# Optimization experiments

Measured on AMD Instinct MI355X. Metric: run time of the kernel, lower is better.

The kernel has to match this reference:

```python
import math
import jax, jax.numpy as jnp
import numpy as np

_INIT_LOG_GAIN = math.log(5.0)
B, L, D = 4, 1024, 256


def setup_inputs() -> dict:
    key = jax.random.key(0)
    kq, kk = jax.random.split(key)
    q = jax.random.normal(kq, (B, L, D), dtype=jnp.float32)
    k = jax.random.normal(kk, (B, L, D), dtype=jnp.float32)
    P_prev = jnp.zeros((B, D, D), dtype=jnp.float32)
    log_gain = jnp.full((D,), _INIT_LOG_GAIN, dtype=jnp.float32)
    output_scale = jnp.ones((D,), dtype=jnp.float32)
    return {"q": q, "k": k, "P_prev": P_prev, "log_gain": log_gain,
            "output_scale": output_scale}


def reference(q, k, P_prev, log_gain, output_scale):
    """Sequential rank-1 projection-state update + normalized matvec + gated tanh.

    q, k: [B, L, D]; P_prev: [B, D, D]. Returns (q_out [B,L,D], P_final [B,D,D]).
    """
    gain = jnp.exp(log_gain)  # effective gain, [D]

    def step(P, qk_t):
        q_t, k_t = qk_t                                   # each [B, D]
        P = P + jnp.einsum('bi,bj->bij', k_t, k_t)        # rank-1 update
        fro = jnp.sqrt(jnp.sum(P * P, axis=(-2, -1), keepdims=True))
        P_norm = P / (fro + 1e-7)
        q_aligned = jnp.einsum('bij,bj->bi', P_norm, q_t)
        q_safe = jnp.tanh(gain * q_aligned) * output_scale
        return P, q_safe

    # scan over the L time axis
    P_final, outs = jax.lax.scan(step, P_prev,
                                 (jnp.swapaxes(q, 0, 1), jnp.swapaxes(k, 0, 1)))
    q_out = jnp.swapaxes(outs, 0, 1)  # [B, L, D]
    return q_out, P_final
```

## Files before the change

kernel.cpp:

```cpp
#include <hip/hip_runtime.h>
#include <math.h>


#define LDSPAD 68

typedef __attribute__((ext_vector_type(8))) short bf16x8;
typedef __attribute__((ext_vector_type(4))) float f32x4;

__device__ __forceinline__ unsigned short f2bf(float x) {
    union { float f; unsigned u; } c; c.f = x;
    return (unsigned short)((c.u + (0x7fffu + ((c.u >> 16) & 1u))) >> 16);
}
__device__ __forceinline__ unsigned f2bf2(float a, float b) {
    union { float f; unsigned u; } ca, cb; ca.f = a; cb.f = b;
    unsigned ua = ca.u + (0x7fffu + ((ca.u >> 16) & 1u));
    unsigned ub = cb.u + (0x7fffu + ((cb.u >> 16) & 1u));
    return (ua >> 16) | (ub & 0xffff0000u);
}
__device__ __forceinline__ void gload16(const unsigned short* g, const unsigned short* l) {
    __builtin_amdgcn_global_load_lds(
        (const __attribute__((address_space(1))) unsigned int*)g,
        (__attribute__((address_space(3))) unsigned int*)l, 16, 0, 0);
}
__device__ __forceinline__ bf16x8 ldsfrag(const unsigned short* lds, int row0, int g0, int lane) {
    int r = row0 + (lane & 15);
    int g = g0 + (lane >> 4);
    return *(const bf16x8*)(lds + r * 64 + (((g ^ (r & 7)) & 7) << 3));
}
#define MFMA16(a, b, c) __builtin_amdgcn_mfma_f32_16x16x32_bf16(a, b, c, 0, 0, 0)

__global__ __launch_bounds__(256) void k_prep(
    const float* __restrict__ Q, const float* __restrict__ K,
    unsigned short* __restrict__ Qb, unsigned short* __restrict__ Kb)
{
    size_t e = ((size_t)blockIdx.x * 256 + threadIdx.x) * 8;
    float4 a0 = *(const float4*)(Q + e), a1 = *(const float4*)(Q + e + 4);
    float4 b0 = *(const float4*)(K + e), b1 = *(const float4*)(K + e + 4);
    uint4 qo = {f2bf2(a0.x, a0.y), f2bf2(a0.z, a0.w), f2bf2(a1.x, a1.y), f2bf2(a1.z, a1.w)};
    uint4 ko = {f2bf2(b0.x, b0.y), f2bf2(b0.z, b0.w), f2bf2(b1.x, b1.y), f2bf2(b1.z, b1.w)};
    *(uint4*)(Qb + e) = qo;
    *(uint4*)(Kb + e) = ko;
}

__global__ __launch_bounds__(256) void k_gsp(
    const unsigned short* __restrict__ Qb, const unsigned short* __restrict__ Kb,
    const float* __restrict__ K, const float* __restrict__ Pprev,
    unsigned short* __restrict__ Sc, float* __restrict__ r2d, float* __restrict__ P4,
    unsigned short* __restrict__ KT, float* __restrict__ basePart,
    int B_, int L, int D, int nT, int nPairs)
{
    __shared__ unsigned short smem[24576];
    int tid = threadIdx.x, lane = tid & 63, w = tid >> 6;
    int fr = lane & 15, fq = lane >> 4;
    int nDt = D >> 6, nLt = L >> 6;
    int nGS = B_ * nPairs;
    int nP4 = B_ * nDt * nDt * 4;
    int nKT = B_ * nLt * nDt;
    int bx = blockIdx.x;
    int id = (bx < nGS) ? ((bx & 7) * (nGS >> 3) + (bx >> 3)) : bx;

    if (id < nGS) {
        int p = id % nPairs;
        int b = id / nPairs;
        int ti = (int)((sqrtf(8.f * p + 1.f) - 1.f) * 0.5f);
        while ((ti + 1) * (ti + 2) / 2 <= p) ti++;
        while (ti * (ti + 1) / 2 > p) ti--;
        int sj = p - ti * (ti + 1) / 2;

        const unsigned short* Qp = Qb + (size_t)b * L * D;
        const unsigned short* Kp = Kb + (size_t)b * L * D;
        int t0 = ti * 64, s0 = sj * 64;
        int wr = w >> 1, wc = w & 1;

        f32x4 g00 = {0,0,0,0}, g01 = {0,0,0,0}, g10 = {0,0,0,0}, g11 = {0,0,0,0};
        f32x4 s00 = {0,0,0,0}, s01 = {0,0,0,0}, s10 = {0,0,0,0}, s11 = {0,0,0,0};

        auto STAGE = [&](int ck, int bo) {
            const unsigned short* Kt = Kp + (size_t)t0 * D + ck * 64;
            const unsigned short* Qt = Qp + (size_t)t0 * D + ck * 64;
            const unsigned short* Ks = Kp + (size_t)s0 * D + ck * 64;
            for (int c = w; c < 8; c += 4) {
                int lrow = c * 8 + (lane >> 3);
                int gof = lrow * D + ((((lane & 7) ^ (lrow & 7)) & 7) << 3);
                gload16(Kt + gof, smem + bo + c * 512);
                gload16(Qt + gof, smem + bo + 4096 + c * 512);
                gload16(Ks + gof, smem + bo + 8192 + c * 512);
            }
        };

        STAGE(0, 0);
        __syncthreads();
        for (int ck = 0; ck < 4; ck++) {
            int cur = (ck & 1) * 12288;
            if (ck < 3) STAGE(ck + 1, 12288 - cur);
            const unsigned short* Kt = smem + cur;
            const unsigned short* Qt = Kt + 4096;
            const unsigned short* Ks = Kt + 8192;
#pragma unroll
            for (int kc = 0; kc < 2; kc++) {
                bf16x8 bK0 = ldsfrag(Ks, wc * 32, kc * 4, lane);
                bf16x8 bK1 = ldsfrag(Ks, wc * 32 + 16, kc * 4, lane);
                bf16x8 aK0 = ldsfrag(Kt, wr * 32, kc * 4, lane);
                bf16x8 aK1 = ldsfrag(Kt, wr * 32 + 16, kc * 4, lane);
                bf16x8 aQ0 = ldsfrag(Qt, wr * 32, kc * 4, lane);
                bf16x8 aQ1 = ldsfrag(Qt, wr * 32 + 16, kc * 4, lane);
                g00 = MFMA16(aK0, bK0, g00);
                g01 = MFMA16(aK0, bK1, g01);
                g10 = MFMA16(aK1, bK0, g10);
                g11 = MFMA16(aK1, bK1, g11);
                s00 = MFMA16(aQ0, bK0, s00);
                s01 = MFMA16(aQ0, bK1, s01);
                s10 = MFMA16(aQ1, bK0, s10);
                s11 = MFMA16(aQ1, bK1, s11);
            }
            __syncthreads();
        }

        float rsv[2][4] = {{0, 0, 0, 0}, {0, 0, 0, 0}};
#define EPI(MI, NI, AG, AS) { _Pragma("unroll") \
        for (int reg = 0; reg < 4; reg++) { \
            int tl = wr * 32 + MI * 16 + fq * 4 + reg; \
            int sl2 = wc * 32 + NI * 16 + fr; \
            int t = ti * 64 + tl, s = sj * 64 + sl2; \
            float g = AG[reg]; \
            float wgt = (s < t) ? 2.f : (s == t ? 1.f : 0.f); \
            rsv[MI][reg] += wgt * g * g; \
            smem[tl * 64 + sl2] = f2bf((s <= t) ? AS[reg] : 0.f); \
        } }
        EPI(0, 0, g00, s00) EPI(0, 1, g01, s01)
        EPI(1, 0, g10, s10) EPI(1, 1, g11, s11)
#undef EPI
        __syncthreads();
        {
            unsigned short* ScT = Sc + ((size_t)(b * nPairs + p) << 12);
            const uint4* s4 = (const uint4*)smem;
            uint4* d4 = (uint4*)ScT;
            d4[tid] = s4[tid];
            d4[tid + 256] = s4[tid + 256];
        }
#pragma unroll
        for (int off = 1; off < 16; off <<= 1) {
#pragma unroll
            for (int mi = 0; mi < 2; mi++)
#pragma unroll
                for (int reg = 0; reg < 4; reg++)
                    rsv[mi][reg] += __shfl_xor(rsv[mi][reg], off);
        }
        if (fr == 0) {
#pragma unroll
            for (int mi = 0; mi < 2; mi++)
#pragma unroll
                for (int reg = 0; reg < 4; reg++) {
                    int t = ti * 64 + wr * 32 + mi * 16 + fq * 4 + reg;
                    r2d[((size_t)(b * 2 * nT) + sj * 2 + wc) * L + t] = rsv[mi][reg];
                }
        }
    } else if (id < nGS + nP4) {
        int id2 = id - nGS;
        int nIJ = nDt * nDt;
        int lc = id2 & 3;
        int ij = (id2 >> 2) % nIJ;
        int b = id2 / (4 * nIJ);
        int ib = (ij / nDt) * 64, jb = (ij % nDt) * 64;
        int tchunk = L >> 2;
        int tstart = lc * tchunk;
        const float* Kf = K + (size_t)b * L * D;
        float* lA = (float*)smem;
        float* lB = lA + 32 * LDSPAD;
        int tx = tid & 15, ty = tid >> 4;
        float acc[4][4] = {};
        for (int tc = 0; tc < tchunk; tc += 32) {
            __syncthreads();
            for (int f = tid; f < 512; f += 256) {
                int r = f >> 4, c4 = (f & 15) * 4;
                *(float4*)&lA[r * LDSPAD + c4] =
                    *(const float4*)(Kf + (size_t)(tstart + tc + r) * D + ib + c4);
                *(float4*)&lB[r * LDSPAD + c4] =
                    *(const float4*)(Kf + (size_t)(tstart + tc + r) * D + jb + c4);
            }
            __syncthreads();
#pragma unroll 8
            for (int t2 = 0; t2 < 32; t2++) {
                float4 av = *(const float4*)&lA[t2 * LDSPAD + ty * 4];
                float4 bv = *(const float4*)&lB[t2 * LDSPAD + tx * 4];
                float aa[4] = {av.x, av.y, av.z, av.w};
                float ba[4] = {bv.x, bv.y, bv.z, bv.w};
#pragma unroll
                for (int i = 0; i < 4; i++)
#pragma unroll
                    for (int j = 0; j < 4; j++) acc[i][j] += aa[i] * ba[j];
            }
        }
        float* dst = P4 + ((((size_t)b * nIJ + ij) * 4 + lc) * 4096);
#pragma unroll
        for (int i = 0; i < 4; i++) {
            float4 o = {acc[i][0], acc[i][1], acc[i][2], acc[i][3]};
            *(float4*)(dst + (ty * 4 + i) * 64 + tx * 4) = o;
        }
    } else if (id < nGS + nP4 + nKT) {
        int id2 = id - nGS - nP4;
        int dt = id2 % nDt, lt = (id2 / nDt) % nLt, b = id2 / (nDt * nLt);
        int l0 = lt * 64, d0 = dt * 64;
        const float* Kf = K + (size_t)b * L * D;
        unsigned short* KTp = KT + (size_t)b * D * L;
        float* lds = (float*)smem;
        int r = tid >> 2, cq = (tid & 3) << 4;
#pragma unroll
        for (int i = 0; i < 16; i += 4) {
            float4 kv = *(const float4*)(Kf + (size_t)(l0 + r) * D + d0 + cq + i);
            lds[r * 65 + cq + i] = kv.x;     lds[r * 65 + cq + i + 1] = kv.y;
            lds[r * 65 + cq + i + 2] = kv.z; lds[r * 65 + cq + i + 3] = kv.w;
        }
        __syncthreads();
        int d2 = tid >> 2, cl = (tid & 3) << 4;
#pragma unroll
        for (int i = 0; i < 16; i += 2) {
            *(unsigned*)(KTp + (size_t)(d0 + d2) * L + l0 + cl + i) =
                f2bf2(lds[(cl + i) * 65 + d2], lds[(cl + i + 1) * 65 + d2]);
        }
    } else {
        int id2 = id - nGS - nP4 - nKT;
        int n = D * D / 16;
        const float* P = Pprev + (size_t)(id2 >> 4) * D * D + (size_t)(id2 & 15) * n;
        float* lds = (float*)smem;
        float s = 0.f;
        for (int i = tid * 4; i < n; i += 1024) {
            float4 vv = *(const float4*)(P + i);
            s += vv.x * vv.x + vv.y * vv.y + vv.z * vv.z + vv.w * vv.w;
        }
#pragma unroll
        for (int off = 32; off; off >>= 1) s += __shfl_down(s, off);
        if (lane == 0) lds[w] = s;
        __syncthreads();
        if (tid == 0) basePart[id2] = lds[0] + lds[1] + lds[2] + lds[3];
    }
}

__global__ __launch_bounds__(256) void k_yp(
    const float* __restrict__ Q, const float* __restrict__ K,
    const float* __restrict__ Pprev, const float* __restrict__ log_gain,
    const float* __restrict__ oscale,
    const unsigned short* __restrict__ Sc, const float* __restrict__ r2d,
    const unsigned short* __restrict__ KT, const float* __restrict__ basePart,
    const float* __restrict__ P4,
    float* __restrict__ out, float* __restrict__ outP,
    int B_, int L, int D, int nT, int nPairs)
{
    __shared__ unsigned short ys[18432];
    __shared__ float invf[1024];
    __shared__ float wred[4];
    int tid = threadIdx.x, lane = tid & 63, w = tid >> 6;
    int fr = lane & 15, fq = lane >> 4;
    int nDt = D >> 6;
    int nDh = 16;
    int nY = B_ * (nT >> 1) * nDh;
    int bx = blockIdx.x;
    int id = (bx < nY) ? ((bx & 7) * (nY >> 3) + (bx >> 3)) : bx;

    if (id < nY) {
        int dh = id % nDh;
        int u = (id / nDh) % (nT >> 1);
        int b = id / (nDh * (nT >> 1));
        int d0 = dh * 16;

        float bb = 0.f;
#pragma unroll
        for (int i = 0; i < 16; i++) bb += basePart[b * 16 + i];

        int t0v = tid * 4;
        int ns = 2 * ((t0v >> 6) + 1);
        float4 vs = {0.f, 0.f, 0.f, 0.f};
        for (int j = 0; j < ns; j++) {
            float4 rr = *(const float4*)&r2d[((size_t)(b * 2 * nT) + j) * L + t0v];
            vs.x += rr.x; vs.y += rr.y; vs.z += rr.z; vs.w += rr.w;
        }
        float v[4] = {vs.x, vs.y, vs.z, vs.w};
        if (bb != 0.f) {
#pragma unroll
            for (int u2 = 0; u2 < 4; u2++) {
                int t = t0v + u2;
                const float* kt = K + ((size_t)b * L + t) * D;
                const float* P = Pprev + (size_t)b * D * D;
                float c = 0.f;
                for (int i = 0; i < D; i++) {
                    float a2 = 0.f;
                    for (int j2 = 0; j2 < D; j2++) a2 += P[i * D + j2] * kt[j2];
                    c += kt[i] * a2;
                }
                v[u2] += 2.f * c;
            }
        }
        v[1] += v[0]; v[2] += v[1]; v[3] += v[2];
        float tot = v[3], sc2 = tot;
        for (int off = 1; off < 64; off <<= 1) {
            float n2 = __shfl_up(sc2, off);
            if (lane >= off) sc2 += n2;
        }
        if (lane == 63) wred[w] = sc2;
        __syncthreads();
        float woff = 0.f;
        for (int i2 = 0; i2 < w; i2++) woff += wred[i2];
        float exc = woff + sc2 - tot;
#pragma unroll
        for (int u2 = 0; u2 < 4; u2++)
            invf[t0v + u2] = 1.f / (sqrtf(bb + exc + v[u2]) + 1e-7f);
        __syncthreads();

        int twl = w << 4;
        int ti0 = u, ti1 = nT - 1 - u;
        int pb0 = ti0 * (ti0 + 1) / 2, pb1 = ti1 * (ti1 + 1) / 2;
        const unsigned short* ScB = Sc + ((size_t)b * nPairs << 12);
        const unsigned short* KTb = KT + (size_t)b * D * L;

        f32x4 c0 = {0, 0, 0, 0};
        f32x4 c1 = {0, 0, 0, 0};

        auto STAGE = [&](int sj, int bo) {
            const unsigned short* T1p = ScB + ((size_t)(pb1 + sj) << 12);
            if (sj <= u) {
                const unsigned short* T0p = ScB + ((size_t)(pb0 + sj) << 12);
                for (int c = w; c < 8; c += 4) {
                    int lrow = c * 8 + (lane >> 3);
                    int go = lrow * 64 + ((((lane & 7) ^ (lrow & 7)) & 7) << 3);
                    gload16(T0p + go, ys + bo + c * 512);
                }
            }
            for (int c = w; c < 8; c += 4) {
                int lrow = c * 8 + (lane >> 3);
                int go = lrow * 64 + ((((lane & 7) ^ (lrow & 7)) & 7) << 3);
                gload16(T1p + go, ys + bo + 4096 + c * 512);
            }
            if (w < 2) {
                int lrow = w * 8 + (lane >> 3);
                int gsw = (((lane & 7) ^ (lrow & 7)) & 7) << 3;
                gload16(KTb + (size_t)(d0 + lrow) * L + sj * 64 + gsw,
                        ys + bo + 8192 + w * 512);
            }
        };

        STAGE(0, 0);
        __syncthreads();
        for (int sj = 0; sj <= ti1; sj++) {
            int cur = (sj & 1) * 9216;
            if (sj < ti1) STAGE(sj + 1, 9216 - cur);
            const unsigned short* S0 = ys + cur;
            const unsigned short* S1 = S0 + 4096;
            const unsigned short* KTl = S0 + 8192;
#pragma unroll
            for (int kc = 0; kc < 2; kc++) {
                bf16x8 b0 = ldsfrag(KTl, 0, kc * 4, lane);
                bf16x8 A1 = ldsfrag(S1, twl, kc * 4, lane);
                c1 = MFMA16(A1, b0, c1);
                if (sj <= ti0) {
                    bf16x8 A0 = ldsfrag(S0, twl, kc * 4, lane);
                    c0 = MFMA16(A0, b0, c0);
                }
            }
            __syncthreads();
        }

        if (bb != 0.f) {
            const float* Qf = Q + (size_t)b * L * D;
            const float* Pb = Pprev + (size_t)b * D * D;
            for (int jj = 0; jj < D; jj++) {
                float p0 = Pb[(size_t)(d0 + fr) * D + jj];
#pragma unroll
                for (int reg = 0; reg < 4; reg++) {
                    float q0v = Qf[(size_t)(ti0 * 64 + twl + fq * 4 + reg) * D + jj];
                    float q1v = Qf[(size_t)(ti1 * 64 + twl + fq * 4 + reg) * D + jj];
                    c0[reg] += q0v * p0;
                    c1[reg] += q1v * p0;
                }
            }
        }

        float gg0 = expf(log_gain[d0 + fr]), os0 = oscale[d0 + fr];
        float* outb = out + (size_t)b * L * D;
#pragma unroll
        for (int reg = 0; reg < 4; reg++) {
            int t0 = ti0 * 64 + twl + fq * 4 + reg;
            int t1 = ti1 * 64 + twl + fq * 4 + reg;
            outb[(size_t)t0 * D + d0 + fr] = tanhf(gg0 * c0[reg] * invf[t0]) * os0;
            outb[(size_t)t1 * D + d0 + fr] = tanhf(gg0 * c1[reg] * invf[t1]) * os0;
        }
    } else {
        int id2 = id - nY;
        int nIJ = nDt * nDt;
        size_t e = ((size_t)id2 * 256 + tid) * 8;
        int b = (int)(e / ((size_t)D * D));
        int rem = (int)(e % ((size_t)D * D));
        int i = rem / D, j = rem % D;
        int ij = (i >> 6) * nDt + (j >> 6);
        int li = i & 63, lj = j & 63;
        const float* src = P4 + ((size_t)b * nIJ + ij) * 4 * 4096 + li * 64 + lj;
        float4 o0 = *(const float4*)(Pprev + e);
        float4 o1 = *(const float4*)(Pprev + e + 4);
#pragma unroll
        for (int lc = 0; lc < 4; lc++) {
            float4 a0 = *(const float4*)(src + lc * 4096);
            float4 a1 = *(const float4*)(src + lc * 4096 + 4);
            o0.x += a0.x; o0.y += a0.y; o0.z += a0.z; o0.w += a0.w;
            o1.x += a1.x; o1.y += a1.y; o1.z += a1.z; o1.w += a1.w;
        }
        *(float4*)(outP + e) = o0;
        *(float4*)(outP + e + 4) = o1;
    }
}

extern "C" void kernel_launch(void* const* d_in, const int* in_sizes, int n_in,
                              void* d_out, int out_size, void* d_ws, size_t ws_size,
                              hipStream_t stream) {
    const float* q = (const float*)d_in[0];
    const float* k = (const float*)d_in[1];
    const float* Pprev = (const float*)d_in[2];
    const float* log_gain = (const float*)d_in[3];
    const float* oscale = (const float*)d_in[4];

    int D = in_sizes[3];
    int B = in_sizes[2] / (D * D);
    int L = in_sizes[0] / (B * D);
    int nT = L / 64;
    int nPairs = nT * (nT + 1) / 2;
    int nDt = D >> 6;
    int nLt = L >> 6;
    int nIJ = nDt * nDt;

    if (D != 256 || L != 1024) return;

    float* out = (float*)d_out;
    float* outP = out + (size_t)B * L * D;

    size_t sR = (size_t)B * L * 2 * nT;
    size_t sBP = 64;
    size_t sP4 = (size_t)B * nIJ * 4 * 4096;
    size_t sSc = (size_t)B * nPairs * 4096;
    size_t sLD = (size_t)B * L * D;
    size_t sKT = (size_t)B * D * L;
    size_t need = (sR + sBP + sP4) * sizeof(float) + (sSc + 2 * sLD + sKT) * 2;
    if (ws_size < need) return;

    float* r2d = (float*)d_ws;
    float* basePart = r2d + sR;
    float* P4 = basePart + sBP;
    unsigned short* Sc = (unsigned short*)(P4 + sP4);
    unsigned short* Qb = Sc + sSc;
    unsigned short* Kb = Qb + sLD;
    unsigned short* KT = Kb + sLD;

    int grid0 = (int)(((size_t)B * L * D) / 2048);
    int grid1 = B * nPairs + B * nIJ * 4 + B * nLt * nDt + B * 16;
    int grid2 = B * (nT >> 1) * 16 + (B * D * D) / 2048;

    k_prep<<<grid0, 256, 0, stream>>>(q, k, Qb, Kb);
    k_gsp<<<grid1, 256, 0, stream>>>(Qb, Kb, k, Pprev, Sc, r2d, P4, KT, basePart,
                                     B, L, D, nT, nPairs);
    k_yp<<<grid2, 256, 0, stream>>>(q, k, Pprev, log_gain, oscale, Sc, r2d, KT,
                                    basePart, P4, out, outP, B, L, D, nT, nPairs);
}
```

Measured before the change: 56.97 us.

## Fuse fp32-to-bf16 conversion into Gram/score kernel, drop prep kernel

Removes the separate k_prep launch that converted Q and K to bf16 in global memory. k_gsp now stages fp32 tiles directly into LDS, in half-width K chunks over twice as many iterations, and converts to bf16 while building MFMA fragments. This saves one kernel launch and the bf16 write/read round trip. In exchange it doubles global and LDS traffic per tile, uses 48KB of LDS (which may lower occupancy), and repeats the conversion across every tile pair that reuses the same rows.

```diff
diff --git a/kernel.cpp b/kernel.cpp
--- a/kernel.cpp
+++ b/kernel.cpp
@@ -17,7 +17,7 @@
     unsigned ub = cb.u + (0x7fffu + ((cb.u >> 16) & 1u));
     return (ua >> 16) | (ub & 0xffff0000u);
 }
-__device__ __forceinline__ void gload16(const unsigned short* g, const unsigned short* l) {
+__device__ __forceinline__ void gload16(const void* g, const void* l) {
     __builtin_amdgcn_global_load_lds(
         (const __attribute__((address_space(1))) unsigned int*)g,
         (__attribute__((address_space(3))) unsigned int*)l, 16, 0, 0);
@@ -27,29 +27,26 @@
     int g = g0 + (lane >> 4);
     return *(const bf16x8*)(lds + r * 64 + (((g ^ (r & 7)) & 7) << 3));
 }
+__device__ __forceinline__ bf16x8 ldsfragf32(const char* tile, int row0, int lane) {
+    int r = row0 + (lane & 15);
+    int g0 = (lane >> 4) << 1;
+    float4 a = *(const float4*)(tile + r * 128 + (((g0 ^ (r & 7)) & 7) << 4));
+    float4 b = *(const float4*)(tile + r * 128 + ((((g0 + 1) ^ (r & 7)) & 7) << 4));
+    union { unsigned u[4]; bf16x8 v; } o;
+    o.u[0] = f2bf2(a.x, a.y); o.u[1] = f2bf2(a.z, a.w);
+    o.u[2] = f2bf2(b.x, b.y); o.u[3] = f2bf2(b.z, b.w);
+    return o.v;
+}
 #define MFMA16(a, b, c) __builtin_amdgcn_mfma_f32_16x16x32_bf16(a, b, c, 0, 0, 0)
 
-__global__ __launch_bounds__(256) void k_prep(
+__global__ __launch_bounds__(256) void k_gsp(
     const float* __restrict__ Q, const float* __restrict__ K,
-    unsigned short* __restrict__ Qb, unsigned short* __restrict__ Kb)
-{
-    size_t e = ((size_t)blockIdx.x * 256 + threadIdx.x) * 8;
-    float4 a0 = *(const float4*)(Q + e), a1 = *(const float4*)(Q + e + 4);
-    float4 b0 = *(const float4*)(K + e), b1 = *(const float4*)(K + e + 4);
-    uint4 qo = {f2bf2(a0.x, a0.y), f2bf2(a0.z, a0.w), f2bf2(a1.x, a1.y), f2bf2(a1.z, a1.w)};
-    uint4 ko = {f2bf2(b0.x, b0.y), f2bf2(b0.z, b0.w), f2bf2(b1.x, b1.y), f2bf2(b1.z, b1.w)};
-    *(uint4*)(Qb + e) = qo;
-    *(uint4*)(Kb + e) = ko;
-}
-
-__global__ __launch_bounds__(256) void k_gsp(
-    const unsigned short* __restrict__ Qb, const unsigned short* __restrict__ Kb,
-    const float* __restrict__ K, const float* __restrict__ Pprev,
+    const float* __restrict__ Pprev,
     unsigned short* __restrict__ Sc, float* __restrict__ r2d, float* __restrict__ P4,
     unsigned short* __restrict__ KT, float* __restrict__ basePart,
     int B_, int L, int D, int nT, int nPairs)
 {
-    __shared__ unsigned short smem[24576];
+    __shared__ char smem[49152];
     int tid = threadIdx.x, lane = tid & 63, w = tid >> 6;
     int fr = lane & 15, fq = lane >> 4;
     int nDt = D >> 6, nLt = L >> 6;
@@ -67,8 +64,8 @@
         while (ti * (ti + 1) / 2 > p) ti--;
         int sj = p - ti * (ti + 1) / 2;
 
-        const unsigned short* Qp = Qb + (size_t)b * L * D;
-        const unsigned short* Kp = Kb + (size_t)b * L * D;
+        const float* Qf = Q + (size_t)b * L * D;
+        const float* Kf = K + (size_t)b * L * D;
         int t0 = ti * 64, s0 = sj * 64;
         int wr = w >> 1, wc = w & 1;
 
@@ -76,47 +73,45 @@
         f32x4 s00 = {0,0,0,0}, s01 = {0,0,0,0}, s10 = {0,0,0,0}, s11 = {0,0,0,0};
 
         auto STAGE = [&](int ck, int bo) {
-            const unsigned short* Kt = Kp + (size_t)t0 * D + ck * 64;
-            const unsigned short* Qt = Qp + (size_t)t0 * D + ck * 64;
-            const unsigned short* Ks = Kp + (size_t)s0 * D + ck * 64;
+            const float* Kt = Kf + (size_t)t0 * D + ck * 32;
+            const float* Qt = Qf + (size_t)t0 * D + ck * 32;
+            const float* Ks = Kf + (size_t)s0 * D + ck * 32;
             for (int c = w; c < 8; c += 4) {
                 int lrow = c * 8 + (lane >> 3);
-                int gof = lrow * D + ((((lane & 7) ^ (lrow & 7)) & 7) << 3);
-                gload16(Kt + gof, smem + bo + c * 512);
-                gload16(Qt + gof, smem + bo + 4096 + c * 512);
-                gload16(Ks + gof, smem + bo + 8192 + c * 512);
+                int gof = lrow * D + ((((lane & 7) ^ (lrow & 7)) & 7) << 2);
+                gload16(Kt + gof, smem + bo + c * 1024);
+                gload16(Qt + gof, smem + bo + 8192 + c * 1024);
+                gload16(Ks + gof, smem + bo + 16384 + c * 1024);
             }
         };
 
         STAGE(0, 0);
         __syncthreads();
-        for (int ck = 0; ck < 4; ck++) {
-            int cur = (ck & 1) * 12288;
-            if (ck < 3) STAGE(ck + 1, 12288 - cur);
-            const unsigned short* Kt = smem + cur;
-            const unsigned short* Qt = Kt + 4096;
-            const unsigned short* Ks = Kt + 8192;
-#pragma unroll
-            for (int kc = 0; kc < 2; kc++) {
-                bf16x8 bK0 = ldsfrag(Ks, wc * 32, kc * 4, lane);
-                bf16x8 bK1 = ldsfrag(Ks, wc * 32 + 16, kc * 4, lane);
-                bf16x8 aK0 = ldsfrag(Kt, wr * 32, kc * 4, lane);
-                bf16x8 aK1 = ldsfrag(Kt, wr * 32 + 16, kc * 4, lane);
-                bf16x8 aQ0 = ldsfrag(Qt, wr * 32, kc * 4, lane);
-                bf16x8 aQ1 = ldsfrag(Qt, wr * 32 + 16, kc * 4, lane);
-                g00 = MFMA16(aK0, bK0, g00);
-                g01 = MFMA16(aK0, bK1, g01);
-                g10 = MFMA16(aK1, bK0, g10);
-                g11 = MFMA16(aK1, bK1, g11);
-                s00 = MFMA16(aQ0, bK0, s00);
-                s01 = MFMA16(aQ0, bK1, s01);
-                s10 = MFMA16(aQ1, bK0, s10);
-                s11 = MFMA16(aQ1, bK1, s11);
-            }
+        for (int ck = 0; ck < 8; ck++) {
+            int cur = (ck & 1) * 24576;
+            if (ck < 7) STAGE(ck + 1, 24576 - cur);
+            const char* Kt = smem + cur;
+            const char* Qt = Kt + 8192;
+            const char* Ks = Kt + 16384;
+            bf16x8 bK0 = ldsfragf32(Ks, wc * 32, lane);
+            bf16x8 bK1 = ldsfragf32(Ks, wc * 32 + 16, lane);
+            bf16x8 aK0 = ldsfragf32(Kt, wr * 32, lane);
+            bf16x8 aK1 = ldsfragf32(Kt, wr * 32 + 16, lane);
+            bf16x8 aQ0 = ldsfragf32(Qt, wr * 32, lane);
+            bf16x8 aQ1 = ldsfragf32(Qt, wr * 32 + 16, lane);
+            g00 = MFMA16(aK0, bK0, g00);
+            g01 = MFMA16(aK0, bK1, g01);
+            g10 = MFMA16(aK1, bK0, g10);
+            g11 = MFMA16(aK1, bK1, g11);
+            s00 = MFMA16(aQ0, bK0, s00);
+            s01 = MFMA16(aQ0, bK1, s01);
+            s10 = MFMA16(aQ1, bK0, s10);
+            s11 = MFMA16(aQ1, bK1, s11);
             __syncthreads();
         }
 
         float rsv[2][4] = {{0, 0, 0, 0}, {0, 0, 0, 0}};
+        unsigned short* sb = (unsigned short*)smem;
 #define EPI(MI, NI, AG, AS) { _Pragma("unroll") \
         for (int reg = 0; reg < 4; reg++) { \
             int tl = wr * 32 + MI * 16 + fq * 4 + reg; \
@@ -125,7 +120,7 @@
             float g = AG[reg]; \
             float wgt = (s < t) ? 2.f : (s == t ? 1.f : 0.f); \
             rsv[MI][reg] += wgt * g * g; \
-            smem[tl * 64 + sl2] = f2bf((s <= t) ? AS[reg] : 0.f); \
+            sb[tl * 64 + sl2] = f2bf((s <= t) ? AS[reg] : 0.f); \
         } }
         EPI(0, 0, g00, s00) EPI(0, 1, g01, s01)
         EPI(1, 0, g10, s10) EPI(1, 1, g11, s11)
@@ -133,7 +128,7 @@
         __syncthreads();
         {
             unsigned short* ScT = Sc + ((size_t)(b * nPairs + p) << 12);
-            const uint4* s4 = (const uint4*)smem;
+            const uint4* s4 = (const uint4*)sb;
             uint4* d4 = (uint4*)ScT;
             d4[tid] = s4[tid];
             d4[tid + 256] = s4[tid + 256];
@@ -434,25 +429,20 @@
     size_t sBP = 64;
     size_t sP4 = (size_t)B * nIJ * 4 * 4096;
     size_t sSc = (size_t)B * nPairs * 4096;
-    size_t sLD = (size_t)B * L * D;
     size_t sKT = (size_t)B * D * L;
-    size_t need = (sR + sBP + sP4) * sizeof(float) + (sSc + 2 * sLD + sKT) * 2;
+    size_t need = (sR + sBP + sP4) * sizeof(float) + (sSc + sKT) * 2;
     if (ws_size < need) return;
 
     float* r2d = (float*)d_ws;
     float* basePart = r2d + sR;
     float* P4 = basePart + sBP;
     unsigned short* Sc = (unsigned short*)(P4 + sP4);
-    unsigned short* Qb = Sc + sSc;
-    unsigned short* Kb = Qb + sLD;
-    unsigned short* KT = Kb + sLD;
-
-    int grid0 = (int)(((size_t)B * L * D) / 2048);
+    unsigned short* KT = Sc + sSc;
+
     int grid1 = B * nPairs + B * nIJ * 4 + B * nLt * nDt + B * 16;
     int grid2 = B * (nT >> 1) * 16 + (B * D * D) / 2048;
 
-    k_prep<<<grid0, 256, 0, stream>>>(q, k, Qb, Kb);
-    k_gsp<<<grid1, 256, 0, stream>>>(Qb, Kb, k, Pprev, Sc, r2d, P4, KT, basePart,
+    k_gsp<<<grid1, 256, 0, stream>>>(q, k, Pprev, Sc, r2d, P4, KT, basePart,
                                      B, L, D, nT, nPairs);
     k_yp<<<grid2, 256, 0, stream>>>(q, k, Pprev, log_gain, oscale, Sc, r2d, KT,
                                     basePart, P4, out, outP, B, L, D, nT, nPairs);
```

After: 56.62 us. No clear change (-0.6%).
